# Kernel tuning notes

Measured on AMD Instinct MI355X. Metric: run time of the kernel, lower is better.

The kernel has to match this reference:

```python
import jax, jax.numpy as jnp
import numpy as np

N, D, E, NNZ = 200000, 128, 1024, 1600000


def setup_inputs() -> dict:
    key = jax.random.key(0)
    ks = jax.random.split(key, 8)
    x = jax.random.normal(ks[0], (N, D), jnp.float32)
    tb_W = jax.random.normal(ks[1], (5, 3, D, D), jnp.float32) * 0.05
    tb_b = jax.random.normal(ks[2], (5, 3, D), jnp.float32) * 0.05
    hg_W = jax.random.normal(ks[3], (2, D, D), jnp.float32) * 0.05
    hg_b = jax.random.normal(ks[4], (2, D), jnp.float32) * 0.05
    hyperedge_attr = jax.random.normal(ks[5], (E, D), jnp.float32)
    node_idx = jax.random.randint(ks[6], (NNZ,), 0, N)
    edge_idx = jax.random.randint(ks[7], (NNZ,), 0, E)
    return dict(x=x, tb_W=tb_W, tb_b=tb_b, hg_W=hg_W, hg_b=hg_b,
                hyperedge_attr=hyperedge_attr, node_idx=node_idx,
                edge_idx=edge_idx, num_hyperedges=E)


def _time_block(x, W, b):
    # 1x1 Conv2d over channel dim == per-node linear. W:[3,D,D], b:[3,D]
    c1 = x @ W[0] + b[0]
    c2 = x @ W[1] + b[1]
    c3 = x @ W[2] + b[2]
    return jax.nn.relu(c1 + jax.nn.sigmoid(c2) + c3)


def _hypergraph_conv(x, node_idx, edge_idx, W, b, num_nodes, num_edges):
    # PyG HypergraphConv, use_attention=False (heads=1):
    # out = D^{-1} H B H^T (x W) + b, H given as COO (node_idx, edge_idx)
    xp = x @ W
    ones = jnp.ones(node_idx.shape[0], xp.dtype)
    Dn = jax.ops.segment_sum(ones, node_idx, num_segments=num_nodes)
    Dn = jnp.where(Dn > 0, 1.0 / Dn, 0.0)
    Be = jax.ops.segment_sum(ones, edge_idx, num_segments=num_edges)
    Be = jnp.where(Be > 0, 1.0 / Be, 0.0)
    # node -> hyperedge aggregation, normalized by 1/B_e
    m = jax.ops.segment_sum(xp[node_idx], edge_idx, num_segments=num_edges) * Be[:, None]
    # hyperedge -> node aggregation, normalized by 1/D_v
    out = jax.ops.segment_sum(m[edge_idx], node_idx, num_segments=num_nodes) * Dn[:, None]
    return out + b


def reference(x, tb_W, tb_b, hg_W, hg_b, hyperedge_attr, node_idx, edge_idx, num_hyperedges):
    # hyperedge_attr is unused when use_attention=False (faithful to PyG)
    n = x.shape[0]
    h = _time_block(x, tb_W[0], tb_b[0])
    h = _hypergraph_conv(h, node_idx, edge_idx, hg_W[0], hg_b[0], n, num_hyperedges)
    h = _time_block(h, tb_W[1], tb_b[1])
    h = _time_block(h, tb_W[2], tb_b[2])
    h = _hypergraph_conv(h, node_idx, edge_idx, hg_W[1], hg_b[1], n, num_hyperedges)
    h = _time_block(h, tb_W[3], tb_b[3])
    h = _time_block(h, tb_W[4], tb_b[4])
    return h
```

## Files before the change

### kernel.cpp

```cpp
#include <hip/hip_runtime.h>
#include <stdint.h>

#define N_NODES 200000
#define DIM     128
#define N_EDGES 1024
#define NNZ_C   1600000
#define NT_TILES 6250

#define NBLK   250
#define CHUNK  6400
#define ITERS  25
#define NCB    196

#define NG_BLOCKS 2048
#define NG_WAVES  (NG_BLOCKS*4)

typedef __attribute__((ext_vector_type(8))) short short8;
typedef __attribute__((ext_vector_type(4))) float f32x4;

__device__ __forceinline__ float u2f(uint32_t u){ union{uint32_t u;float f;} x; x.u=u; return x.f; }
__device__ __forceinline__ uint32_t f2u(float f){ union{uint32_t u;float f;} x; x.f=f; return x.u; }
__device__ __forceinline__ unsigned short f2bf(float f){
  uint32_t u = f2u(f);
  u += 0x7fffu + ((u >> 16) & 1u);
  return (unsigned short)(u >> 16);
}

__global__ void prep_tb_w(const float* __restrict__ W, short* __restrict__ Wt){
  int i = blockIdx.x*256 + threadIdx.x;
  if (i >= 5*384*128) return;
  int k   = i & 127;
  int col = (i >> 7) % 384;
  int s   = i / 49152;
  int j = col >> 7, n = col & 127;
  Wt[i] = (short)f2bf(W[((s*3 + j)*128 + k)*128 + n]);
}
__global__ void prep_hg_wf(const float* __restrict__ W, float* __restrict__ Wtf){
  int i = blockIdx.x*256 + threadIdx.x;
  if (i >= 2*128*128) return;
  int k = i & 127;
  int n = (i >> 7) & 127;
  int g = i >> 14;
  Wtf[i] = W[(g*128 + k)*128 + n];
}

__global__ __launch_bounds__(256) void hist_kernel(
    const int* __restrict__ nidx, const int* __restrict__ eidx,
    int* __restrict__ ebh, int* __restrict__ nbh)
{
  __shared__ int eh[N_EDGES];
  __shared__ int nh[NCB];
  int tid = threadIdx.x, blk = blockIdx.x;
  #pragma unroll
  for (int l = tid; l < N_EDGES; l += 256) eh[l] = 0;
  for (int l = tid; l < NCB; l += 256) nh[l] = 0;
  __syncthreads();
  int base = blk*CHUNK;
  for (int it = 0; it < ITERS; it++){
    int i = base + it*256 + tid;
    atomicAdd(&eh[eidx[i]], 1);
    atomicAdd(&nh[nidx[i] >> 10], 1);
  }
  __syncthreads();
  for (int l = tid; l < N_EDGES; l += 256) ebh[blk*N_EDGES + l] = eh[l];
  for (int l = tid; l < NCB; l += 256) nbh[blk*NCB + l] = nh[l];
}

__global__ __launch_bounds__(1024) void escan_kernel(
    int* __restrict__ ebh, int* __restrict__ eoff)
{
  __shared__ int sc[1024];
  int e = threadIdx.x;
  int total = 0;
  #pragma unroll 10
  for (int b = 0; b < NBLK; b++){
    int idx = b*N_EDGES + e;
    int t = ebh[idx];
    ebh[idx] = total;
    total += t;
  }
  sc[e] = total; __syncthreads();
  for (int off=1; off<1024; off<<=1){
    int v = (e >= off) ? sc[e-off] : 0;
    __syncthreads();
    sc[e] += v;
    __syncthreads();
  }
  int base = sc[e] - total;
  eoff[e] = base;
  if (e == 1023) eoff[1024] = sc[1023];
  #pragma unroll 10
  for (int b = 0; b < NBLK; b++) ebh[b*N_EDGES + e] += base;
}

__global__ __launch_bounds__(256) void nscan_kernel(
    int* __restrict__ nbh, int* __restrict__ cbase)
{
  __shared__ int sc[256];
  int c = threadIdx.x;
  int total = 0;
  if (c < NCB){
    #pragma unroll 10
    for (int b = 0; b < NBLK; b++){
      int idx = b*NCB + c;
      int t = nbh[idx];
      nbh[idx] = total;
      total += t;
    }
  }
  sc[c] = (c < NCB) ? total : 0; __syncthreads();
  for (int off=1; off<256; off<<=1){
    int v = (c >= off) ? sc[c-off] : 0;
    __syncthreads();
    sc[c] += v;
    __syncthreads();
  }
  int base = sc[c] - ((c < NCB) ? total : 0);
  if (c < NCB) cbase[c] = base;
  if (c == NCB-1) cbase[NCB] = sc[c];
  __syncthreads();
  if (c < NCB){
    #pragma unroll 10
    for (int b = 0; b < NBLK; b++) nbh[b*NCB + c] += base;
  }
}

__global__ __launch_bounds__(256) void scatter_kernel(
    const int* __restrict__ nidx, const int* __restrict__ eidx,
    const int* __restrict__ ebh, const int* __restrict__ nbh,
    int* __restrict__ enodes, uint32_t* __restrict__ pairs)
{
  __shared__ int cure[N_EDGES];
  __shared__ int curn[NCB];
  int tid = threadIdx.x, blk = blockIdx.x;
  for (int l = tid; l < N_EDGES; l += 256) cure[l] = ebh[blk*N_EDGES + l];
  for (int l = tid; l < NCB; l += 256)     curn[l] = nbh[blk*NCB + l];
  __syncthreads();
  int base = blk*CHUNK;
  for (int it = 0; it < ITERS; it++){
    int i = base + it*256 + tid;
    int v = nidx[i], e = eidx[i];
    int pe = atomicAdd(&cure[e], 1);
    enodes[pe] = v;
    int pn = atomicAdd(&curn[v >> 10], 1);
    pairs[pn] = ((uint32_t)v << 10) | (uint32_t)e;
  }
}

__global__ __launch_bounds__(256) void node_build_kernel(
    const uint32_t* __restrict__ pairs, const int* __restrict__ cbase,
    int* __restrict__ noff, int* __restrict__ nedges)
{
  __shared__ int cnt[1024];
  __shared__ int off[1024];
  __shared__ int part[256];
  int tid = threadIdx.x, c = blockIdx.x;
  int n0 = c << 10;
  int nloc = min(1024, N_NODES - n0);
  int s = cbase[c], e = cbase[c+1];
  #pragma unroll
  for (int l = tid; l < 1024; l += 256) cnt[l] = 0;
  __syncthreads();
  for (int i = s + tid; i < e; i += 256)
    atomicAdd(&cnt[(pairs[i] >> 10) & 1023], 1);
  __syncthreads();
  int c0 = cnt[tid*4], c1 = cnt[tid*4+1], c2 = cnt[tid*4+2], c3 = cnt[tid*4+3];
  int sum = c0+c1+c2+c3;
  part[tid] = sum; __syncthreads();
  for (int o=1; o<256; o<<=1){
    int v = (tid >= o) ? part[tid-o] : 0;
    __syncthreads();
    part[tid] += v;
    __syncthreads();
  }
  int pb = part[tid] - sum;
  off[tid*4]   = pb;
  off[tid*4+1] = pb + c0;
  off[tid*4+2] = pb + c0 + c1;
  off[tid*4+3] = pb + c0 + c1 + c2;
  __syncthreads();
  for (int l = tid; l < nloc; l += 256) noff[n0 + l] = s + off[l];
  if (c == 0 && tid == 0) noff[N_NODES] = NNZ_C;
  __syncthreads();
  for (int i = s + tid; i < e; i += 256){
    uint32_t p = pairs[i];
    int local = (p >> 10) & 1023;
    int pos = s + atomicAdd(&off[local], 1);
    nedges[pos] = (int)(p & 1023);
  }
}

template<bool IN_F32, int OUT_MODE>
__global__ __launch_bounds__(256, 2) void gemm_kernel(
    const void* __restrict__ in, void* __restrict__ out,
    const short* __restrict__ Wt, const float* __restrict__ bias)
{
  __shared__ short Atile[32][136];
  const int tid  = threadIdx.x;
  const int lane = tid & 63;
  const int w    = tid >> 6;
  const int l15  = lane & 15;
  const int quad = lane >> 4;

  short8 bfrag[3][2][4];
  #pragma unroll
  for (int j = 0; j < 3; j++)
    #pragma unroll
    for (int nt = 0; nt < 2; nt++){
      const short* bp = Wt + (j*128 + w*32 + nt*16 + l15)*128 + quad*8;
      #pragma unroll
      for (int ks = 0; ks < 4; ks++)
        bfrag[j][nt][ks] = *(const short8*)(bp + ks*32);
    }

  float bv[3][2];
  #pragma unroll
  for (int j = 0; j < 3; j++)
    #pragma unroll
    for (int nt = 0; nt < 2; nt++)
      bv[j][nt] = bias[j*128 + w*32 + nt*16 + l15];

  const int arow = tid >> 3;
  const int aseg = (tid & 7) * 2;

  short8 pre0, pre1;
  auto loadA = [&](int t){
    int off = (t*32 + arow)*128 + aseg*8;
    if (IN_F32){
      const float* f = (const float*)in + off;
      f32x4 q0 = ((const f32x4*)f)[0];
      f32x4 q1 = ((const f32x4*)f)[1];
      f32x4 q2 = ((const f32x4*)f)[2];
      f32x4 q3 = ((const f32x4*)f)[3];
      short8 t0, t1;
      #pragma unroll
      for (int u = 0; u < 4; u++){
        t0[u]   = (short)f2bf(q0[u]);
        t0[u+4] = (short)f2bf(q1[u]);
        t1[u]   = (short)f2bf(q2[u]);
        t1[u+4] = (short)f2bf(q3[u]);
      }
      pre0 = t0; pre1 = t1;
    } else {
      const short* hp = (const short*)in + off;
      pre0 = *(const short8*)hp;
      pre1 = *(const short8*)(hp + 8);
    }
  };

  int t = blockIdx.x;
  loadA(t);
  for (;;){
    __syncthreads();
    *(short8*)&Atile[arow][aseg*8]     = pre0;
    *(short8*)&Atile[arow][aseg*8 + 8] = pre1;
    __syncthreads();
    int tn = t + gridDim.x;
    if (tn < NT_TILES) loadA(tn);

    const int base = t*32;
    #pragma unroll
    for (int rt = 0; rt < 2; rt++){
      short8 af[4];
      #pragma unroll
      for (int ks = 0; ks < 4; ks++)
        af[ks] = *(const short8*)&Atile[rt*16 + l15][ks*32 + quad*8];

      f32x4 acc[3][2];
      #pragma unroll
      for (int j = 0; j < 3; j++)
        #pragma unroll
        for (int nt = 0; nt < 2; nt++){
          acc[j][nt] = (f32x4){0.f, 0.f, 0.f, 0.f};
          #pragma unroll
          for (int ks = 0; ks < 4; ks++)
            acc[j][nt] = __builtin_amdgcn_mfma_f32_16x16x32_bf16(
                af[ks], bfrag[j][nt][ks], acc[j][nt], 0, 0, 0);
        }

      #pragma unroll
      for (int nt = 0; nt < 2; nt++){
        int col = w*32 + nt*16 + l15;
        #pragma unroll
        for (int r = 0; r < 4; r++){
          int row = base + rt*16 + quad*4 + r;
          float c2 = acc[1][nt][r] + bv[1][nt];
          float sg = 1.f / (1.f + __expf(-c2));
          float v = acc[0][nt][r] + bv[0][nt] + sg + acc[2][nt][r] + bv[2][nt];
          v = fmaxf(v, 0.f);
          if (OUT_MODE == 1) ((float*)out)[row*128 + col] = v;
          else if (OUT_MODE == 0) ((unsigned short*)out)[row*128 + col] = f2bf(v);
          else {
            int pk = __builtin_amdgcn_cvt_pk_fp8_f32(v, v, 0, false);
            ((unsigned char*)out)[row*128 + col] = (unsigned char)(pk & 0xff);
          }
        }
      }
    }
    if (tn >= NT_TILES) break;
    t = tn;
  }
}

__device__ __forceinline__ void acc16(float* a, uint4 r){
  uint32_t w[4] = {r.x, r.y, r.z, r.w};
  #pragma unroll
  for (int q = 0; q < 4; q++){
    auto lo = __builtin_amdgcn_cvt_pk_f32_fp8(w[q], false);
    auto hi = __builtin_amdgcn_cvt_pk_f32_fp8(w[q], true);
    a[q*4+0] += lo[0]; a[q*4+1] += lo[1]; a[q*4+2] += hi[0]; a[q*4+3] += hi[1];
  }
}

__global__ __launch_bounds__(256) void edge_gather_kernel(
    const unsigned char* __restrict__ h8, const int* __restrict__ eoff,
    const int* __restrict__ enodes, float* __restrict__ s_e)
{
  int e = blockIdx.x;
  int s = eoff[e], en = eoff[e+1];
  int tid  = threadIdx.x;
  int slot = tid >> 3;
  int ch   = tid & 7;
  const size_t choff = (size_t)ch * 16;

  float a[16];
  #pragma unroll
  for (int j = 0; j < 16; j++) a[j] = 0.f;

  int i0 = s + slot;
  int n0 = (i0      < en) ? enodes[i0]      : -1;
  int n1 = (i0 + 32 < en) ? enodes[i0 + 32] : -1;
  int n2 = (i0 + 64 < en) ? enodes[i0 + 64] : -1;
  int n3 = (i0 + 96 < en) ? enodes[i0 + 96] : -1;

  while (i0 < en){
    int i1 = i0 + 128;
    int m0 = (i1      < en) ? enodes[i1]      : -1;
    int m1 = (i1 + 32 < en) ? enodes[i1 + 32] : -1;
    int m2 = (i1 + 64 < en) ? enodes[i1 + 64] : -1;
    int m3 = (i1 + 96 < en) ? enodes[i1 + 96] : -1;

    uint4 r0 = *(const uint4*)(h8 + (((size_t)max(n0,0)) << 7) + choff);
    uint4 r1 = *(const uint4*)(h8 + (((size_t)max(n1,0)) << 7) + choff);
    uint4 r2 = *(const uint4*)(h8 + (((size_t)max(n2,0)) << 7) + choff);
    uint4 r3 = *(const uint4*)(h8 + (((size_t)max(n3,0)) << 7) + choff);
    if (n0 < 0) r0 = make_uint4(0,0,0,0);
    if (n1 < 0) r1 = make_uint4(0,0,0,0);
    if (n2 < 0) r2 = make_uint4(0,0,0,0);
    if (n3 < 0) r3 = make_uint4(0,0,0,0);

    acc16(a, r0); acc16(a, r1); acc16(a, r2); acc16(a, r3);

    n0 = m0; n1 = m1; n2 = m2; n3 = m3;
    i0 = i1;
  }

  __shared__ float red[32][132];
  #pragma unroll
  for (int j = 0; j < 16; j++) red[slot][ch*16 + j] = a[j];
  __syncthreads();
  if (tid < 128){
    float sum = 0.f;
    #pragma unroll
    for (int r = 0; r < 32; r++) sum += red[r][tid];
    s_e[e*128 + tid] = sum;
  }
}

__global__ __launch_bounds__(128) void egemm_kernel(
    const float* __restrict__ s_e, const int* __restrict__ eoff,
    const float* __restrict__ Wtf, uint32_t* __restrict__ mbf)
{
  __shared__ float srow[128];
  __shared__ float sacc[128];
  int e = blockIdx.x, n = threadIdx.x;
  srow[n] = s_e[e*128 + n];
  __syncthreads();
  int deg = eoff[e+1] - eoff[e];
  float be = deg > 0 ? 1.f/(float)deg : 0.f;
  const f32x4* w4 = (const f32x4*)(Wtf + n*128);
  float acc = 0.f;
  #pragma unroll
  for (int k = 0; k < 32; k++){
    f32x4 qv = w4[k];
    acc += qv[0]*srow[k*4] + qv[1]*srow[k*4+1] + qv[2]*srow[k*4+2] + qv[3]*srow[k*4+3];
  }
  sacc[n] = acc * be;
  __syncthreads();
  if (n < 64){
    uint32_t lo = f2bf(sacc[2*n]);
    uint32_t hi = f2bf(sacc[2*n+1]);
    mbf[e*64 + n] = (hi << 16) | lo;
  }
}

__global__ __launch_bounds__(256) void node_gather_kernel(
    const uint32_t* __restrict__ mbf, const int* __restrict__ noff,
    const int* __restrict__ nedges, const float* __restrict__ hb,
    uint32_t* __restrict__ outp)
{
  int wid  = (blockIdx.x << 2) | (threadIdx.x >> 6);
  int lane = threadIdx.x & 63;
  float b0 = hb[2*lane], b1 = hb[2*lane+1];
  const int K = (N_NODES + NG_WAVES - 1) / NG_WAVES;
  int v0 = wid * K;
  int v1 = min(v0 + K, N_NODES);
  for (int v = v0; v < v1; v++){
    int s = noff[v], e = noff[v+1];
    float a0 = 0.f, a1 = 0.f, a2 = 0.f, a3 = 0.f;
    int i = s;
    for (; i + 4 <= e; i += 4){
      int e0 = nedges[i],   e1 = nedges[i+1];
      int e2 = nedges[i+2], e3 = nedges[i+3];
      uint32_t r0 = mbf[(e0 << 6) | lane];
      uint32_t r1 = mbf[(e1 << 6) | lane];
      uint32_t r2 = mbf[(e2 << 6) | lane];
      uint32_t r3 = mbf[(e3 << 6) | lane];
      a0 += u2f(r0 << 16); a1 += u2f(r0 & 0xffff0000u);
      a2 += u2f(r1 << 16); a3 += u2f(r1 & 0xffff0000u);
      a0 += u2f(r2 << 16); a1 += u2f(r2 & 0xffff0000u);
      a2 += u2f(r3 << 16); a3 += u2f(r3 & 0xffff0000u);
    }
    for (; i < e; i++){
      int ed = nedges[i];
      uint32_t r = mbf[(ed << 6) | lane];
      a0 += u2f(r << 16); a1 += u2f(r & 0xffff0000u);
    }
    a0 += a2; a1 += a3;
    float dn = (e > s) ? 1.f/(float)(e - s) : 0.f;
    uint32_t lo = f2bf(a0*dn + b0);
    uint32_t hi = f2bf(a1*dn + b1);
    outp[((size_t)v << 6) | lane] = (hi << 16) | lo;
  }
}

extern "C" void kernel_launch(void* const* d_in, const int* in_sizes, int n_in,
                              void* d_out, int out_size, void* d_ws, size_t ws_size,
                              hipStream_t stream)
{
  (void)in_sizes; (void)n_in; (void)out_size; (void)ws_size;
  const float* x   = (const float*)d_in[0];
  const float* tbW = (const float*)d_in[1];
  const float* tbb = (const float*)d_in[2];
  const float* hgW = (const float*)d_in[3];
  const float* hgb = (const float*)d_in[4];
  const int* nidx  = (const int*)d_in[6];
  const int* eidx  = (const int*)d_in[7];
  float* out = (float*)d_out;

  char* p = (char*)d_ws;
  auto alloc = [&](size_t sz){ void* r = (void*)p; p += (sz + 255) & ~(size_t)255; return r; };
  unsigned short* hA = (unsigned short*)alloc((size_t)N_NODES*DIM*2);
  unsigned short* hB = (unsigned short*)alloc((size_t)N_NODES*DIM*2);
  unsigned char*  h8 = (unsigned char*)alloc((size_t)N_NODES*DIM);
  float* s_e  = (float*)alloc((size_t)N_EDGES*DIM*4);
  uint32_t* mbf = (uint32_t*)alloc((size_t)N_EDGES*64*4);
  short* WtTb = (short*)alloc((size_t)5*384*128*2);
  float* Wtf  = (float*)alloc((size_t)2*128*128*4);
  int* ebh  = (int*)alloc((size_t)NBLK*N_EDGES*4);
  int* nbh  = (int*)alloc((size_t)NBLK*NCB*4);
  int* eoff = (int*)alloc((N_EDGES+1)*4);
  int* cbase= (int*)alloc((NCB+1)*4);
  int* noff = (int*)alloc((size_t)(N_NODES+1)*4);
  int* enodes = (int*)alloc((size_t)NNZ_C*4);
  int* nedges = (int*)alloc((size_t)NNZ_C*4);
  uint32_t* pairs = (uint32_t*)h8;

  prep_tb_w<<<960, 256, 0, stream>>>(tbW, WtTb);
  prep_hg_wf<<<128, 256, 0, stream>>>(hgW, Wtf);

  hist_kernel<<<NBLK, 256, 0, stream>>>(nidx, eidx, ebh, nbh);
  escan_kernel<<<1, 1024, 0, stream>>>(ebh, eoff);
  nscan_kernel<<<1, 256, 0, stream>>>(nbh, cbase);
  scatter_kernel<<<NBLK, 256, 0, stream>>>(nidx, eidx, ebh, nbh, enodes, pairs);
  node_build_kernel<<<NCB, 256, 0, stream>>>(pairs, cbase, noff, nedges);

  gemm_kernel<true, 2><<<1024, 256, 0, stream>>>(x, h8, WtTb, tbb);
  edge_gather_kernel<<<N_EDGES, 256, 0, stream>>>(h8, eoff, enodes, s_e);
  egemm_kernel<<<N_EDGES, 128, 0, stream>>>(s_e, eoff, Wtf, mbf);
  node_gather_kernel<<<NG_BLOCKS, 256, 0, stream>>>(mbf, noff, nedges, hgb, (uint32_t*)hA);
  gemm_kernel<false, 0><<<1024, 256, 0, stream>>>(hA, hB, WtTb + 1*49152, tbb + 1*384);
  gemm_kernel<false, 2><<<1024, 256, 0, stream>>>(hB, h8, WtTb + 2*49152, tbb + 2*384);
  edge_gather_kernel<<<N_EDGES, 256, 0, stream>>>(h8, eoff, enodes, s_e);
  egemm_kernel<<<N_EDGES, 128, 0, stream>>>(s_e, eoff, Wtf + 16384, mbf);
  node_gather_kernel<<<NG_BLOCKS, 256, 0, stream>>>(mbf, noff, nedges, hgb + 128, (uint32_t*)hA);
  gemm_kernel<false, 0><<<1024, 256, 0, stream>>>(hA, hB, WtTb + 3*49152, tbb + 3*384);
  gemm_kernel<false, 1><<<1024, 256, 0, stream>>>(hB, out, WtTb + 4*49152, tbb + 4*384);
}
```

Before: 681.4 us.

## Fuse hyperedge-to-node gather into the following time-block GEMM A-tile load

Removes the separate node_gather kernel and its bf16 intermediate hA. The GEMM's A-tile loader now gathers fp32 hyperedge messages per node through the CSR, normalizes by degree, adds the conv bias and converts to bf16 on the fly. egemm now writes fp32 messages instead of packed bf16. This saves one kernel launch and a 51MB write+read round trip per conv, but adds irregular gathers inside the GEMM prefetch that may stall the MFMA pipeline and doubles message bytes per gather.

```diff
diff --git a/kernel.cpp b/kernel.cpp
--- a/kernel.cpp
+++ b/kernel.cpp
@@ -11,9 +11,6 @@
 #define CHUNK  6400
 #define ITERS  25
 #define NCB    196
-
-#define NG_BLOCKS 2048
-#define NG_WAVES  (NG_BLOCKS*4)
 
 typedef __attribute__((ext_vector_type(8))) short short8;
 typedef __attribute__((ext_vector_type(4))) float f32x4;
@@ -190,10 +187,12 @@
   }
 }
 
-template<bool IN_F32, int OUT_MODE>
+template<int IN_MODE, int OUT_MODE>
 __global__ __launch_bounds__(256, 2) void gemm_kernel(
     const void* __restrict__ in, void* __restrict__ out,
-    const short* __restrict__ Wt, const float* __restrict__ bias)
+    const short* __restrict__ Wt, const float* __restrict__ bias,
+    const int* __restrict__ noff, const int* __restrict__ nedges,
+    const float* __restrict__ hb)
 {
   __shared__ short Atile[32][136];
   const int tid  = threadIdx.x;
@@ -223,10 +222,17 @@
   const int arow = tid >> 3;
   const int aseg = (tid & 7) * 2;
 
+  f32x4 hbv[4];
+  if (IN_MODE == 2){
+    const f32x4* hb4 = (const f32x4*)hb + (tid & 7)*4;
+    #pragma unroll
+    for (int q = 0; q < 4; q++) hbv[q] = hb4[q];
+  }
+
   short8 pre0, pre1;
   auto loadA = [&](int t){
     int off = (t*32 + arow)*128 + aseg*8;
-    if (IN_F32){
+    if (IN_MODE == 1){
       const float* f = (const float*)in + off;
       f32x4 q0 = ((const f32x4*)f)[0];
       f32x4 q1 = ((const f32x4*)f)[1];
@@ -241,10 +247,40 @@
         t1[u+4] = (short)f2bf(q3[u]);
       }
       pre0 = t0; pre1 = t1;
-    } else {
+    } else if (IN_MODE == 0){
       const short* hp = (const short*)in + off;
       pre0 = *(const short8*)hp;
       pre1 = *(const short8*)(hp + 8);
+    } else {
+      int v = t*32 + arow;
+      int s = noff[v], e = noff[v+1];
+      f32x4 a0 = (f32x4){0,0,0,0}, a1 = a0, a2 = a0, a3 = a0;
+      const f32x4* mf4 = (const f32x4*)in;
+      const int segf = (tid & 7)*4;
+      int i = s;
+      for (; i + 2 <= e; i += 2){
+        int e0 = nedges[i], e1 = nedges[i+1];
+        const f32x4* r0 = mf4 + (e0 << 5) + segf;
+        const f32x4* r1 = mf4 + (e1 << 5) + segf;
+        f32x4 p0 = r0[0], p1 = r0[1], p2 = r0[2], p3 = r0[3];
+        f32x4 q0 = r1[0], q1 = r1[1], q2 = r1[2], q3 = r1[3];
+        a0 += p0; a1 += p1; a2 += p2; a3 += p3;
+        a0 += q0; a1 += q1; a2 += q2; a3 += q3;
+      }
+      if (i < e){
+        const f32x4* r0 = mf4 + (nedges[i] << 5) + segf;
+        a0 += r0[0]; a1 += r0[1]; a2 += r0[2]; a3 += r0[3];
+      }
+      float dn = (e > s) ? 1.f/(float)(e - s) : 0.f;
+      short8 t0, t1;
+      #pragma unroll
+      for (int u = 0; u < 4; u++){
+        t0[u]   = (short)f2bf(a0[u]*dn + hbv[0][u]);
+        t0[u+4] = (short)f2bf(a1[u]*dn + hbv[1][u]);
+        t1[u]   = (short)f2bf(a2[u]*dn + hbv[2][u]);
+        t1[u+4] = (short)f2bf(a3[u]*dn + hbv[3][u]);
+      }
+      pre0 = t0; pre1 = t1;
     }
   };
 
@@ -369,10 +405,9 @@
 
 __global__ __launch_bounds__(128) void egemm_kernel(
     const float* __restrict__ s_e, const int* __restrict__ eoff,
-    const float* __restrict__ Wtf, uint32_t* __restrict__ mbf)
+    const float* __restrict__ Wtf, float* __restrict__ mf)
 {
   __shared__ float srow[128];
-  __shared__ float sacc[128];
   int e = blockIdx.x, n = threadIdx.x;
   srow[n] = s_e[e*128 + n];
   __syncthreads();
@@ -385,53 +420,7 @@
     f32x4 qv = w4[k];
     acc += qv[0]*srow[k*4] + qv[1]*srow[k*4+1] + qv[2]*srow[k*4+2] + qv[3]*srow[k*4+3];
   }
-  sacc[n] = acc * be;
-  __syncthreads();
-  if (n < 64){
-    uint32_t lo = f2bf(sacc[2*n]);
-    uint32_t hi = f2bf(sacc[2*n+1]);
-    mbf[e*64 + n] = (hi << 16) | lo;
-  }
-}
-
-__global__ __launch_bounds__(256) void node_gather_kernel(
-    const uint32_t* __restrict__ mbf, const int* __restrict__ noff,
-    const int* __restrict__ nedges, const float* __restrict__ hb,
-    uint32_t* __restrict__ outp)
-{
-  int wid  = (blockIdx.x << 2) | (threadIdx.x >> 6);
-  int lane = threadIdx.x & 63;
-  float b0 = hb[2*lane], b1 = hb[2*lane+1];
-  const int K = (N_NODES + NG_WAVES - 1) / NG_WAVES;
-  int v0 = wid * K;
-  int v1 = min(v0 + K, N_NODES);
-  for (int v = v0; v < v1; v++){
-    int s = noff[v], e = noff[v+1];
-    float a0 = 0.f, a1 = 0.f, a2 = 0.f, a3 = 0.f;
-    int i = s;
-    for (; i + 4 <= e; i += 4){
-      int e0 = nedges[i],   e1 = nedges[i+1];
-      int e2 = nedges[i+2], e3 = nedges[i+3];
-      uint32_t r0 = mbf[(e0 << 6) | lane];
-      uint32_t r1 = mbf[(e1 << 6) | lane];
-      uint32_t r2 = mbf[(e2 << 6) | lane];
-      uint32_t r3 = mbf[(e3 << 6) | lane];
-      a0 += u2f(r0 << 16); a1 += u2f(r0 & 0xffff0000u);
-      a2 += u2f(r1 << 16); a3 += u2f(r1 & 0xffff0000u);
-      a0 += u2f(r2 << 16); a1 += u2f(r2 & 0xffff0000u);
-      a2 += u2f(r3 << 16); a3 += u2f(r3 & 0xffff0000u);
-    }
-    for (; i < e; i++){
-      int ed = nedges[i];
-      uint32_t r = mbf[(ed << 6) | lane];
-      a0 += u2f(r << 16); a1 += u2f(r & 0xffff0000u);
-    }
-    a0 += a2; a1 += a3;
-    float dn = (e > s) ? 1.f/(float)(e - s) : 0.f;
-    uint32_t lo = f2bf(a0*dn + b0);
-    uint32_t hi = f2bf(a1*dn + b1);
-    outp[((size_t)v << 6) | lane] = (hi << 16) | lo;
-  }
+  mf[e*128 + n] = acc * be;
 }
 
 extern "C" void kernel_launch(void* const* d_in, const int* in_sizes, int n_in,
@@ -450,11 +439,10 @@
 
   char* p = (char*)d_ws;
   auto alloc = [&](size_t sz){ void* r = (void*)p; p += (sz + 255) & ~(size_t)255; return r; };
-  unsigned short* hA = (unsigned short*)alloc((size_t)N_NODES*DIM*2);
   unsigned short* hB = (unsigned short*)alloc((size_t)N_NODES*DIM*2);
   unsigned char*  h8 = (unsigned char*)alloc((size_t)N_NODES*DIM);
   float* s_e  = (float*)alloc((size_t)N_EDGES*DIM*4);
-  uint32_t* mbf = (uint32_t*)alloc((size_t)N_EDGES*64*4);
+  float* mf   = (float*)alloc((size_t)N_EDGES*DIM*4);
   short* WtTb = (short*)alloc((size_t)5*384*128*2);
   float* Wtf  = (float*)alloc((size_t)2*128*128*4);
   int* ebh  = (int*)alloc((size_t)NBLK*N_EDGES*4);
@@ -475,15 +463,18 @@
   scatter_kernel<<<NBLK, 256, 0, stream>>>(nidx, eidx, ebh, nbh, enodes, pairs);
   node_build_kernel<<<NCB, 256, 0, stream>>>(pairs, cbase, noff, nedges);
 
-  gemm_kernel<true, 2><<<1024, 256, 0, stream>>>(x, h8, WtTb, tbb);
+  gemm_kernel<1, 2><<<1024, 256, 0, stream>>>(x, h8, WtTb, tbb,
+                                              nullptr, nullptr, nullptr);
   edge_gather_kernel<<<N_EDGES, 256, 0, stream>>>(h8, eoff, enodes, s_e);
-  egemm_kernel<<<N_EDGES, 128, 0, stream>>>(s_e, eoff, Wtf, mbf);
-  node_gather_kernel<<<NG_BLOCKS, 256, 0, stream>>>(mbf, noff, nedges, hgb, (uint32_t*)hA);
-  gemm_kernel<false, 0><<<1024, 256, 0, stream>>>(hA, hB, WtTb + 1*49152, tbb + 1*384);
-  gemm_kernel<false, 2><<<1024, 256, 0, stream>>>(hB, h8, WtTb + 2*49152, tbb + 2*384);
+  egemm_kernel<<<N_EDGES, 128, 0, stream>>>(s_e, eoff, Wtf, mf);
+  gemm_kernel<2, 0><<<1024, 256, 0, stream>>>(mf, hB, WtTb + 1*49152, tbb + 1*384,
+                                              noff, nedges, hgb);
+  gemm_kernel<0, 2><<<1024, 256, 0, stream>>>(hB, h8, WtTb + 2*49152, tbb + 2*384,
+                                              nullptr, nullptr, nullptr);
   edge_gather_kernel<<<N_EDGES, 256, 0, stream>>>(h8, eoff, enodes, s_e);
-  egemm_kernel<<<N_EDGES, 128, 0, stream>>>(s_e, eoff, Wtf + 16384, mbf);
-  node_gather_kernel<<<NG_BLOCKS, 256, 0, stream>>>(mbf, noff, nedges, hgb + 128, (uint32_t*)hA);
-  gemm_kernel<false, 0><<<1024, 256, 0, stream>>>(hA, hB, WtTb + 3*49152, tbb + 3*384);
-  gemm_kernel<false, 1><<<1024, 256, 0, stream>>>(hB, out, WtTb + 4*49152, tbb + 4*384);
-}
+  egemm_kernel<<<N_EDGES, 128, 0, stream>>>(s_e, eoff, Wtf + 16384, mf);
+  gemm_kernel<2, 0><<<1024, 256, 0, stream>>>(mf, hB, WtTb + 3*49152, tbb + 3*384,
+                                              noff, nedges, hgb + 128);
+  gemm_kernel<0, 1><<<1024, 256, 0, stream>>>(hB, out, WtTb + 4*49152, tbb + 4*384,
+                                              nullptr, nullptr, nullptr);
+}
```

New measurement: 710.6 us. +4.3%, slower.

## Flatten node gather into continuous software-pipelined edge stream per wave

Applied to the files above, without the earlier changes.

The node gather kernel now treats each wave's node range as one continuous stream of CSR entries. It prefetches the next four hyperedge rows while accumulating the current four, and flushes node outputs at row boundaries, so short rows of about 8 entries no longer stall on per-node loop setup. Edge indices are stored pre-shifted by 6 in the CSR build, which removes a shift from the inner loop. The cost is more branching on boundary checks and serial accumulation into two accumulators instead of four.

```diff
diff --git a/kernel.cpp b/kernel.cpp
--- a/kernel.cpp
+++ b/kernel.cpp
@@ -186,7 +186,7 @@
     uint32_t p = pairs[i];
     int local = (p >> 10) & 1023;
     int pos = s + atomicAdd(&off[local], 1);
-    nedges[pos] = (int)(p & 1023);
+    nedges[pos] = (int)((p & 1023) << 6);
   }
 }
 
@@ -405,33 +405,49 @@
   const int K = (N_NODES + NG_WAVES - 1) / NG_WAVES;
   int v0 = wid * K;
   int v1 = min(v0 + K, N_NODES);
-  for (int v = v0; v < v1; v++){
-    int s = noff[v], e = noff[v+1];
-    float a0 = 0.f, a1 = 0.f, a2 = 0.f, a3 = 0.f;
-    int i = s;
-    for (; i + 4 <= e; i += 4){
-      int e0 = nedges[i],   e1 = nedges[i+1];
-      int e2 = nedges[i+2], e3 = nedges[i+3];
-      uint32_t r0 = mbf[(e0 << 6) | lane];
-      uint32_t r1 = mbf[(e1 << 6) | lane];
-      uint32_t r2 = mbf[(e2 << 6) | lane];
-      uint32_t r3 = mbf[(e3 << 6) | lane];
-      a0 += u2f(r0 << 16); a1 += u2f(r0 & 0xffff0000u);
-      a2 += u2f(r1 << 16); a3 += u2f(r1 & 0xffff0000u);
-      a0 += u2f(r2 << 16); a1 += u2f(r2 & 0xffff0000u);
-      a2 += u2f(r3 << 16); a3 += u2f(r3 & 0xffff0000u);
-    }
-    for (; i < e; i++){
-      int ed = nedges[i];
-      uint32_t r = mbf[(ed << 6) | lane];
-      a0 += u2f(r << 16); a1 += u2f(r & 0xffff0000u);
-    }
-    a0 += a2; a1 += a3;
-    float dn = (e > s) ? 1.f/(float)(e - s) : 0.f;
+  if (v0 >= v1) return;
+  int s    = noff[v0];
+  int send = noff[v1];
+
+  int v   = v0;
+  int vs  = s;
+  int bnd = noff[v0+1];
+  float a0 = 0.f, a1 = 0.f;
+
+  auto flush = [&](int iend){
+    float dn = (iend > vs) ? 1.f/(float)(iend - vs) : 0.f;
     uint32_t lo = f2bf(a0*dn + b0);
     uint32_t hi = f2bf(a1*dn + b1);
     outp[((size_t)v << 6) | lane] = (hi << 16) | lo;
-  }
+    a0 = 0.f; a1 = 0.f;
+    vs = iend;
+    v++;
+    bnd = (v < v1) ? noff[v+1] : 0x7fffffff;
+  };
+
+  uint32_t r0 = (s     < send) ? mbf[nedges[s]     + lane] : 0u;
+  uint32_t r1 = (s + 1 < send) ? mbf[nedges[s + 1] + lane] : 0u;
+  uint32_t r2 = (s + 2 < send) ? mbf[nedges[s + 2] + lane] : 0u;
+  uint32_t r3 = (s + 3 < send) ? mbf[nedges[s + 3] + lane] : 0u;
+
+  for (int ii = s; ii < send; ii += 4){
+    uint32_t q0 = (ii + 4 < send) ? mbf[nedges[ii + 4] + lane] : 0u;
+    uint32_t q1 = (ii + 5 < send) ? mbf[nedges[ii + 5] + lane] : 0u;
+    uint32_t q2 = (ii + 6 < send) ? mbf[nedges[ii + 6] + lane] : 0u;
+    uint32_t q3 = (ii + 7 < send) ? mbf[nedges[ii + 7] + lane] : 0u;
+
+    { while (bnd == ii) flush(ii);
+      a0 += u2f(r0 << 16); a1 += u2f(r0 & 0xffff0000u); }
+    if (ii + 1 < send){ while (bnd == ii + 1) flush(ii + 1);
+      a0 += u2f(r1 << 16); a1 += u2f(r1 & 0xffff0000u); }
+    if (ii + 2 < send){ while (bnd == ii + 2) flush(ii + 2);
+      a0 += u2f(r2 << 16); a1 += u2f(r2 & 0xffff0000u); }
+    if (ii + 3 < send){ while (bnd == ii + 3) flush(ii + 3);
+      a0 += u2f(r3 << 16); a1 += u2f(r3 & 0xffff0000u); }
+
+    r0 = q0; r1 = q1; r2 = q2; r3 = q3;
+  }
+  while (v < v1) flush(send);
 }
 
 extern "C" void kernel_launch(void* const* d_in, const int* in_sizes, int n_in,
```

Result: slower. 714.8 us (+4.9%).

## Store hyperedge messages as fp32 and software-pipeline the node gather loop

Applied to the files above, without the earlier changes.

The egemm kernel now writes per-edge messages as fp32 rows instead of packed bf16, which removes a shared-memory round trip and the unpack arithmetic in the node gather. nedges is prestored with the row offset already shifted, so each gather is a single float2 load per lane. The node gather prefetches the next four edge indices while accumulating the current ones, reads CSR offsets as wave-uniform scalars and reuses the previous end offset. It also launches twice as many blocks. The message table doubles in size, to 512KB, which should still fit in cache, and per-node loads double in bytes.

```diff
diff --git a/kernel.cpp b/kernel.cpp
--- a/kernel.cpp
+++ b/kernel.cpp
@@ -12,7 +12,7 @@
 #define ITERS  25
 #define NCB    196
 
-#define NG_BLOCKS 2048
+#define NG_BLOCKS 4096
 #define NG_WAVES  (NG_BLOCKS*4)
 
 typedef __attribute__((ext_vector_type(8))) short short8;
@@ -186,7 +186,7 @@
     uint32_t p = pairs[i];
     int local = (p >> 10) & 1023;
     int pos = s + atomicAdd(&off[local], 1);
-    nedges[pos] = (int)(p & 1023);
+    nedges[pos] = (int)((p & 1023) << 6);
   }
 }
 
@@ -369,10 +369,9 @@
 
 __global__ __launch_bounds__(128) void egemm_kernel(
     const float* __restrict__ s_e, const int* __restrict__ eoff,
-    const float* __restrict__ Wtf, uint32_t* __restrict__ mbf)
+    const float* __restrict__ Wtf, float* __restrict__ mf)
 {
   __shared__ float srow[128];
-  __shared__ float sacc[128];
   int e = blockIdx.x, n = threadIdx.x;
   srow[n] = s_e[e*128 + n];
   __syncthreads();
@@ -385,52 +384,53 @@
     f32x4 qv = w4[k];
     acc += qv[0]*srow[k*4] + qv[1]*srow[k*4+1] + qv[2]*srow[k*4+2] + qv[3]*srow[k*4+3];
   }
-  sacc[n] = acc * be;
-  __syncthreads();
-  if (n < 64){
-    uint32_t lo = f2bf(sacc[2*n]);
-    uint32_t hi = f2bf(sacc[2*n+1]);
-    mbf[e*64 + n] = (hi << 16) | lo;
-  }
+  mf[e*128 + n] = acc * be;
 }
 
 __global__ __launch_bounds__(256) void node_gather_kernel(
-    const uint32_t* __restrict__ mbf, const int* __restrict__ noff,
+    const float* __restrict__ mf, const int* __restrict__ noff,
     const int* __restrict__ nedges, const float* __restrict__ hb,
     uint32_t* __restrict__ outp)
 {
   int wid  = (blockIdx.x << 2) | (threadIdx.x >> 6);
   int lane = threadIdx.x & 63;
+  const float2* mfp = (const float2*)mf + lane;
   float b0 = hb[2*lane], b1 = hb[2*lane+1];
   const int K = (N_NODES + NG_WAVES - 1) / NG_WAVES;
   int v0 = wid * K;
   int v1 = min(v0 + K, N_NODES);
+  if (v0 >= v1) return;
+
+  int s = __builtin_amdgcn_readfirstlane(noff[v0]);
   for (int v = v0; v < v1; v++){
-    int s = noff[v], e = noff[v+1];
+    int e = __builtin_amdgcn_readfirstlane(noff[v+1]);
     float a0 = 0.f, a1 = 0.f, a2 = 0.f, a3 = 0.f;
     int i = s;
-    for (; i + 4 <= e; i += 4){
-      int e0 = nedges[i],   e1 = nedges[i+1];
-      int e2 = nedges[i+2], e3 = nedges[i+3];
-      uint32_t r0 = mbf[(e0 << 6) | lane];
-      uint32_t r1 = mbf[(e1 << 6) | lane];
-      uint32_t r2 = mbf[(e2 << 6) | lane];
-      uint32_t r3 = mbf[(e3 << 6) | lane];
-      a0 += u2f(r0 << 16); a1 += u2f(r0 & 0xffff0000u);
-      a2 += u2f(r1 << 16); a3 += u2f(r1 & 0xffff0000u);
-      a0 += u2f(r2 << 16); a1 += u2f(r2 & 0xffff0000u);
-      a2 += u2f(r3 << 16); a3 += u2f(r3 & 0xffff0000u);
+    int em4 = e - 4;
+    if (i <= em4){
+      int e0 = nedges[i], e1 = nedges[i+1], e2 = nedges[i+2], e3 = nedges[i+3];
+      for (; i <= em4; i += 4){
+        int j = min(i + 4, em4);
+        int p0 = nedges[j], p1 = nedges[j+1], p2 = nedges[j+2], p3 = nedges[j+3];
+        float2 r0 = mfp[e0];
+        float2 r1 = mfp[e1];
+        float2 r2 = mfp[e2];
+        float2 r3 = mfp[e3];
+        a0 += r0.x; a1 += r0.y; a2 += r1.x; a3 += r1.y;
+        a0 += r2.x; a1 += r2.y; a2 += r3.x; a3 += r3.y;
+        e0 = p0; e1 = p1; e2 = p2; e3 = p3;
+      }
     }
     for (; i < e; i++){
-      int ed = nedges[i];
-      uint32_t r = mbf[(ed << 6) | lane];
-      a0 += u2f(r << 16); a1 += u2f(r & 0xffff0000u);
+      float2 r = mfp[nedges[i]];
+      a0 += r.x; a1 += r.y;
     }
     a0 += a2; a1 += a3;
     float dn = (e > s) ? 1.f/(float)(e - s) : 0.f;
     uint32_t lo = f2bf(a0*dn + b0);
     uint32_t hi = f2bf(a1*dn + b1);
     outp[((size_t)v << 6) | lane] = (hi << 16) | lo;
+    s = e;
   }
 }
 
@@ -454,7 +454,7 @@
   unsigned short* hB = (unsigned short*)alloc((size_t)N_NODES*DIM*2);
   unsigned char*  h8 = (unsigned char*)alloc((size_t)N_NODES*DIM);
   float* s_e  = (float*)alloc((size_t)N_EDGES*DIM*4);
-  uint32_t* mbf = (uint32_t*)alloc((size_t)N_EDGES*64*4);
+  float* mf   = (float*)alloc((size_t)N_EDGES*DIM*4);
   short* WtTb = (short*)alloc((size_t)5*384*128*2);
   float* Wtf  = (float*)alloc((size_t)2*128*128*4);
   int* ebh  = (int*)alloc((size_t)NBLK*N_EDGES*4);
@@ -477,13 +477,13 @@
 
   gemm_kernel<true, 2><<<1024, 256, 0, stream>>>(x, h8, WtTb, tbb);
   edge_gather_kernel<<<N_EDGES, 256, 0, stream>>>(h8, eoff, enodes, s_e);
-  egemm_kernel<<<N_EDGES, 128, 0, stream>>>(s_e, eoff, Wtf, mbf);
-  node_gather_kernel<<<NG_BLOCKS, 256, 0, stream>>>(mbf, noff, nedges, hgb, (uint32_t*)hA);
+  egemm_kernel<<<N_EDGES, 128, 0, stream>>>(s_e, eoff, Wtf, mf);
+  node_gather_kernel<<<NG_BLOCKS, 256, 0, stream>>>(mf, noff, nedges, hgb, (uint32_t*)hA);
   gemm_kernel<false, 0><<<1024, 256, 0, stream>>>(hA, hB, WtTb + 1*49152, tbb + 1*384);
   gemm_kernel<false, 2><<<1024, 256, 0, stream>>>(hB, h8, WtTb + 2*49152, tbb + 2*384);
   edge_gather_kernel<<<N_EDGES, 256, 0, stream>>>(h8, eoff, enodes, s_e);
-  egemm_kernel<<<N_EDGES, 128, 0, stream>>>(s_e, eoff, Wtf + 16384, mbf);
-  node_gather_kernel<<<NG_BLOCKS, 256, 0, stream>>>(mbf, noff, nedges, hgb + 128, (uint32_t*)hA);
+  egemm_kernel<<<N_EDGES, 128, 0, stream>>>(s_e, eoff, Wtf + 16384, mf);
+  node_gather_kernel<<<NG_BLOCKS, 256, 0, stream>>>(mf, noff, nedges, hgb + 128, (uint32_t*)hA);
   gemm_kernel<false, 0><<<1024, 256, 0, stream>>>(hA, hB, WtTb + 3*49152, tbb + 3*384);
   gemm_kernel<false, 1><<<1024, 256, 0, stream>>>(hB, out, WtTb + 4*49152, tbb + 4*384);
 }
```

Result: no change. 674.0 us (-1.1%).
